# Performance work log

Hardware: AMD Instinct MI355X
Metric: run time of the kernel (lower is better)

The kernel has to match this reference:

```python
import jax, jax.numpy as jnp
import numpy as np

U_DIM = 2048
V_DIM = 2048
LATENT = 2048
BATCH = 8192
SLOPE = 0.001  # LeakyReLU negative slope
EPS = 1e-5     # torch LayerNorm default eps


def layer_norm(x, gamma, beta):
    mu = jnp.mean(x, axis=-1, keepdims=True)
    var = jnp.var(x, axis=-1, keepdims=True)
    return (x - mu) * jax.lax.rsqrt(var + EPS) * gamma + beta


def leaky_relu(x):
    return jnp.where(x >= 0, x, SLOPE * x)


def setup_inputs() -> dict:
    key = jax.random.key(0)
    ks = jax.random.split(key, 6)
    u = jax.random.normal(ks[0], (BATCH, V_DIM), dtype=jnp.float32)
    v = jax.random.normal(ks[1], (BATCH, U_DIM), dtype=jnp.float32)
    # LayerNorm affine params (torch default: weight=1, bias=0 at init; randomize slightly)
    ln_u_w = jnp.ones((V_DIM,), jnp.float32)
    ln_u_b = jnp.zeros((V_DIM,), jnp.float32)
    ln_v_w = jnp.ones((U_DIM,), jnp.float32)
    ln_v_b = jnp.zeros((U_DIM,), jnp.float32)
    # Linear params (Kaiming-uniform-like scale)
    su = 1.0 / np.sqrt(V_DIM)
    sv = 1.0 / np.sqrt(U_DIM)
    W_u = jax.random.uniform(ks[2], (V_DIM, LATENT), jnp.float32, -su, su)
    b_u = jax.random.uniform(ks[3], (LATENT,), jnp.float32, -su, su)
    W_v = jax.random.uniform(ks[4], (U_DIM, LATENT), jnp.float32, -sv, sv)
    b_v = jax.random.uniform(ks[5], (LATENT,), jnp.float32, -sv, sv)
    return {"u": u, "v": v, "ln_u_w": ln_u_w, "ln_u_b": ln_u_b,
            "ln_v_w": ln_v_w, "ln_v_b": ln_v_b,
            "W_u": W_u, "b_u": b_u, "W_v": W_v, "b_v": b_v}


def reference(u, v, ln_u_w, ln_u_b, ln_v_w, ln_v_b, W_u, b_u, W_v, b_v):
    # u tower: LayerNorm -> Linear -> LeakyReLU
    hu = leaky_relu(layer_norm(u, ln_u_w, ln_u_b) @ W_u + b_u)   # [B, latent]
    # v tower: LayerNorm -> Linear -> LeakyReLU
    hv = leaky_relu(layer_norm(v, ln_v_w, ln_v_b) @ W_v + b_v)   # [B, latent]
    # dot-product reduction per row
    return jnp.sum(hu * hv, axis=-1)                              # [B]
```

## Files before the change

kernel.cpp:

```cpp
#include <hip/hip_runtime.h>

typedef unsigned short u16;
typedef __attribute__((ext_vector_type(8))) short short8;
typedef __attribute__((ext_vector_type(16))) float f32x16;

#define DIM 2048
#define NROWS 8192
#define SLOPE 0.001f
#define LN_EPS 1e-5f

#define LN_BLOCKS 4096
#define WT_BLOCKS 2048

#define BM 128
#define BN 256
#define BK 64
#define NT (DIM / BK)

__device__ __forceinline__ u16 f2bf(float f) {
    unsigned int u = __float_as_uint(f);
    u += 0x7FFFu + ((u >> 16) & 1u);
    return (u16)(u >> 16);
}

__device__ __forceinline__ void gload_lds16(const void* g, void* l) {
    __builtin_amdgcn_global_load_lds(
        (const __attribute__((address_space(1))) void*)g,
        (__attribute__((address_space(3))) void*)l, 16, 0, 0);
}

__global__ __launch_bounds__(256) void prep_kernel(
    const float* __restrict__ u, const float* __restrict__ v,
    const float* __restrict__ lnu_w, const float* __restrict__ lnu_b,
    const float* __restrict__ lnv_w, const float* __restrict__ lnv_b,
    const float* __restrict__ Wu, const float* __restrict__ Wv,
    u16* __restrict__ Au, u16* __restrict__ Av,
    u16* __restrict__ WtU, u16* __restrict__ WtV)
{
    __shared__ u16 tile[64][66];

    if (blockIdx.x < LN_BLOCKS) {
        const int wave = threadIdx.x >> 6;
        const int lane = threadIdx.x & 63;
        const int r = blockIdx.x * 4 + wave;
        const bool isv = r >= NROWS;
        const int row = isv ? (r - NROWS) : r;
        const float* __restrict__ src = (isv ? v : u) + (size_t)row * DIM;
        const float* __restrict__ gw = isv ? lnv_w : lnu_w;
        const float* __restrict__ gb = isv ? lnv_b : lnu_b;
        u16* __restrict__ dst = (isv ? Av : Au) + (size_t)row * DIM;

        float4 x[8];
        #pragma unroll
        for (int i = 0; i < 8; ++i)
            x[i] = *(const float4*)(src + i * 256 + lane * 4);

        float s = 0.f, s2 = 0.f;
        #pragma unroll
        for (int i = 0; i < 8; ++i) {
            s  += (x[i].x + x[i].y) + (x[i].z + x[i].w);
            s2 += x[i].x*x[i].x + x[i].y*x[i].y + x[i].z*x[i].z + x[i].w*x[i].w;
        }
        #pragma unroll
        for (int m = 1; m < 64; m <<= 1) {
            s  += __shfl_xor(s, m);
            s2 += __shfl_xor(s2, m);
        }
        const float mu = s * (1.0f / DIM);
        const float rstd = rsqrtf(s2 * (1.0f / DIM) - mu * mu + LN_EPS);

        #pragma unroll
        for (int i = 0; i < 8; ++i) {
            const float4 w4 = *(const float4*)(gw + i * 256 + lane * 4);
            const float4 b4 = *(const float4*)(gb + i * 256 + lane * 4);
            union { u16 us[4]; uint2 v2; } pk;
            pk.us[0] = f2bf((x[i].x - mu) * rstd * w4.x + b4.x);
            pk.us[1] = f2bf((x[i].y - mu) * rstd * w4.y + b4.y);
            pk.us[2] = f2bf((x[i].z - mu) * rstd * w4.z + b4.z);
            pk.us[3] = f2bf((x[i].w - mu) * rstd * w4.w + b4.w);
            *(uint2*)(dst + i * 256 + lane * 4) = pk.v2;
        }
    } else {
        const int b = blockIdx.x - LN_BLOCKS;
        const int tower = b >> 10;
        const int t6 = b & 1023;
        const int n0 = (t6 & 31) * 64;
        const int k0 = (t6 >> 5) * 64;
        const float* __restrict__ src = tower ? Wv : Wu;
        u16* __restrict__ dst = tower ? WtV : WtU;
        const int c  = threadIdx.x & 15;
        const int rq = threadIdx.x >> 4;

        #pragma unroll
        for (int i = 0; i < 4; ++i) {
            const int k = rq + 16 * i;
            const float4 w = *(const float4*)(src + (size_t)(k0 + k) * DIM + n0 + c * 4);
            union { u16 us[4]; uint2 v2; } pk;
            pk.us[0] = f2bf(w.x); pk.us[1] = f2bf(w.y);
            pk.us[2] = f2bf(w.z); pk.us[3] = f2bf(w.w);
            *(uint2*)&tile[k][c * 4] = pk.v2;
        }
        __syncthreads();
        #pragma unroll
        for (int i = 0; i < 4; ++i) {
            const int n = rq + 16 * i;
            union { u16 us[4]; uint2 v2; } pk;
            #pragma unroll
            for (int j = 0; j < 4; ++j) pk.us[j] = tile[c * 4 + j][n];
            *(uint2*)(dst + (size_t)(n0 + n) * DIM + k0 + c * 4) = pk.v2;
        }
    }
}

__global__ __launch_bounds__(512) void fused_gemm_dot(
    const u16* __restrict__ Au, const u16* __restrict__ Av,
    const u16* __restrict__ WtU, const u16* __restrict__ WtV,
    const float* __restrict__ b_u, const float* __restrict__ b_v,
    float* __restrict__ out)
{
    __shared__ __align__(16) u16 smA[3][BM * BK];
    __shared__ __align__(16) u16 smB[3][BN * BK];

    const int tid   = threadIdx.x;
    const int wave  = tid >> 6;
    const int lane  = tid & 63;
    const int l31   = lane & 31;
    const int khalf = lane >> 5;
    const int wr    = wave >> 2;
    const int wc    = wave & 3;
    const int srow  = lane >> 3;
    const int gsw   = ((lane & 7) ^ srow ^ wave) * 8;

    const size_t arow0 = (size_t)blockIdx.x * BM;
    const size_t ncol0 = (size_t)blockIdx.y * BN;

#define STAGE(Asrc, Bsrc, k0, bi) do {                                             \
        _Pragma("unroll")                                                          \
        for (int i_ = 0; i_ < 2; ++i_) {                                           \
            const int rg_ = i_ * 64 + wave * 8;                                    \
            gload_lds16((Asrc) + (size_t)(rg_ + srow) * DIM + (k0) + gsw,          \
                        &smA[bi][rg_ * BK]);                                       \
        }                                                                          \
        _Pragma("unroll")                                                          \
        for (int i_ = 0; i_ < 4; ++i_) {                                           \
            const int rg_ = i_ * 64 + wave * 8;                                    \
            gload_lds16((Bsrc) + (size_t)(rg_ + srow) * DIM + (k0) + gsw,          \
                        &smB[bi][rg_ * BK]);                                       \
        }                                                                          \
    } while (0)

#define PHASE(bi, KS0) do {                                                        \
        const u16* sa_ = &smA[bi][0];                                              \
        const u16* sb_ = &smB[bi][0];                                              \
        short8 af_[2][2], bf_[2][2];                                               \
        _Pragma("unroll")                                                          \
        for (int kk_ = 0; kk_ < 2; ++kk_) {                                        \
            const int cb_ = ((KS0) + kk_) * 2 + khalf;                             \
            _Pragma("unroll")                                                      \
            for (int mi_ = 0; mi_ < 2; ++mi_) {                                    \
                const int row_ = wr * 64 + mi_ * 32 + l31;                         \
                const int sl_ = cb_ ^ (row_ & 7) ^ ((row_ >> 3) & 7);              \
                af_[mi_][kk_] = *(const short8*)(sa_ + row_ * BK + sl_ * 8);       \
            }                                                                      \
            _Pragma("unroll")                                                      \
            for (int ni_ = 0; ni_ < 2; ++ni_) {                                    \
                const int row_ = wc * 64 + ni_ * 32 + l31;                         \
                const int sl_ = cb_ ^ (row_ & 7) ^ ((row_ >> 3) & 7);              \
                bf_[ni_][kk_] = *(const short8*)(sb_ + row_ * BK + sl_ * 8);       \
            }                                                                      \
        }                                                                          \
        __builtin_amdgcn_s_setprio(1);                                             \
        _Pragma("unroll")                                                          \
        for (int kk_ = 0; kk_ < 2; ++kk_)                                          \
            _Pragma("unroll")                                                      \
            for (int mi_ = 0; mi_ < 2; ++mi_)                                      \
                _Pragma("unroll")                                                  \
                for (int ni_ = 0; ni_ < 2; ++ni_)                                  \
                    acc[mi_][ni_] = __builtin_amdgcn_mfma_f32_32x32x16_bf16(       \
                        af_[mi_][kk_], bf_[ni_][kk_], acc[mi_][ni_], 0, 0, 0);     \
        __builtin_amdgcn_s_setprio(0);                                             \
    } while (0)

    f32x16 acc[2][2];
    unsigned int hu_pk[2][2][8];

    #pragma unroll
    for (int tower = 0; tower < 2; ++tower) {
        const u16* __restrict__ Asrc = (tower ? Av : Au) + arow0 * DIM;
        const u16* __restrict__ Bsrc = (tower ? WtV : WtU) + ncol0 * DIM;

        #pragma unroll
        for (int mi = 0; mi < 2; ++mi)
            #pragma unroll
            for (int ni = 0; ni < 2; ++ni)
                #pragma unroll
                for (int r = 0; r < 16; ++r)
                    acc[mi][ni][r] = 0.f;

        STAGE(Asrc, Bsrc, 0, 0);
        STAGE(Asrc, Bsrc, BK, 1);

        int cur = 0;
        for (int t = 0; t < NT; ++t) {
            __builtin_amdgcn_sched_barrier(0);
            __builtin_amdgcn_s_barrier();
            __builtin_amdgcn_sched_barrier(0);
            if (t + 2 < NT) {
                int nb = cur + 2; if (nb >= 3) nb -= 3;
                STAGE(Asrc, Bsrc, (t + 2) * BK, nb);
                asm volatile("s_waitcnt vmcnt(12)" ::: "memory");
            } else if (t + 2 == NT) {
                asm volatile("s_waitcnt vmcnt(6)" ::: "memory");
            } else {
                asm volatile("s_waitcnt vmcnt(0)" ::: "memory");
            }
            __builtin_amdgcn_s_barrier();
            PHASE(cur, 0);
            __builtin_amdgcn_s_barrier();
            PHASE(cur, 2);
            cur = (cur == 2) ? 0 : cur + 1;
        }

        if (tower == 0) {
            #pragma unroll
            for (int ni = 0; ni < 2; ++ni) {
                const float bias = b_u[ncol0 + wc * 64 + ni * 32 + l31];
                #pragma unroll
                for (int mi = 0; mi < 2; ++mi) {
                    #pragma unroll
                    for (int p = 0; p < 8; ++p) {
                        float h0 = acc[mi][ni][p * 2] + bias;
                        float h1 = acc[mi][ni][p * 2 + 1] + bias;
                        h0 = h0 >= 0.f ? h0 : SLOPE * h0;
                        h1 = h1 >= 0.f ? h1 : SLOPE * h1;
                        hu_pk[mi][ni][p] = (unsigned)f2bf(h0) | ((unsigned)f2bf(h1) << 16);
                    }
                }
            }
        }
    }

    #pragma unroll
    for (int mi = 0; mi < 2; ++mi) {
        #pragma unroll
        for (int rg = 0; rg < 4; ++rg) {
            float rsum[4] = {0.f, 0.f, 0.f, 0.f};
            #pragma unroll
            for (int ni = 0; ni < 2; ++ni) {
                const float bias = b_v[ncol0 + wc * 64 + ni * 32 + l31];
                #pragma unroll
                for (int r = 0; r < 4; ++r) {
                    const int reg = rg * 4 + r;
                    float hv = acc[mi][ni][reg] + bias;
                    hv = hv >= 0.f ? hv : SLOPE * hv;
                    const unsigned pk = hu_pk[mi][ni][reg >> 1];
                    const unsigned bits = (reg & 1) ? (pk & 0xFFFF0000u) : (pk << 16);
                    rsum[r] += __uint_as_float(bits) * hv;
                }
            }
            #pragma unroll
            for (int r = 0; r < 4; ++r) {
                const int reg = rg * 4 + r;
                float vsum = rsum[r];
                vsum += __shfl_xor(vsum, 1);
                vsum += __shfl_xor(vsum, 2);
                vsum += __shfl_xor(vsum, 4);
                vsum += __shfl_xor(vsum, 8);
                vsum += __shfl_xor(vsum, 16);
                if (l31 == 0) {
                    const int row = (int)arow0 + wr * 64 + mi * 32
                                  + (reg & 3) + 8 * (reg >> 2) + 4 * khalf;
                    atomicAdd(out + row, vsum);
                }
            }
        }
    }
#undef STAGE
#undef PHASE
}

extern "C" void kernel_launch(void* const* d_in, const int* in_sizes, int n_in,
                              void* d_out, int out_size, void* d_ws, size_t ws_size,
                              hipStream_t stream)
{
    const float* u     = (const float*)d_in[0];
    const float* v     = (const float*)d_in[1];
    const float* lnu_w = (const float*)d_in[2];
    const float* lnu_b = (const float*)d_in[3];
    const float* lnv_w = (const float*)d_in[4];
    const float* lnv_b = (const float*)d_in[5];
    const float* W_u   = (const float*)d_in[6];
    const float* b_u   = (const float*)d_in[7];
    const float* W_v   = (const float*)d_in[8];
    const float* b_v   = (const float*)d_in[9];
    float* out = (float*)d_out;

    char* ws = (char*)d_ws;
    u16* Au  = (u16*)(ws);
    u16* Av  = (u16*)(ws + (size_t)NROWS * DIM * 2);
    u16* WtU = (u16*)(ws + (size_t)NROWS * DIM * 4);
    u16* WtV = (u16*)(ws + (size_t)NROWS * DIM * 4 + (size_t)DIM * DIM * 2);

    hipMemsetAsync(d_out, 0, (size_t)out_size * sizeof(float), stream);
    prep_kernel<<<LN_BLOCKS + WT_BLOCKS, 256, 0, stream>>>(
        u, v, lnu_w, lnu_b, lnv_w, lnv_b, W_u, W_v, Au, Av, WtU, WtV);
    fused_gemm_dot<<<dim3(NROWS / BM, DIM / BN), 512, 0, stream>>>(
        Au, Av, WtU, WtV, b_u, b_v, out);
}
```

Baseline: 368.3 us.

## Pipeline loads across both towers and fold output zeroing into prep kernel

The two tower K-loops now share one global tile index, so prefetches for the v tower start during the tail of the u tower and the pipeline never drains between towers. Global-to-LDS staging for the next tile is split into two halves and interleaved with the fragment reads and MFMA phases, and the waitcnt is simplified to a constant depth. The separate hipMemsetAsync of the output is removed; the prep kernel zeroes it instead, saving one launch. The risk is correctness at the tower boundary, since buffer rotation and the waitcnt counts must stay consistent with the staggered staging.

```diff
diff --git a/kernel.cpp b/kernel.cpp
--- a/kernel.cpp
+++ b/kernel.cpp
@@ -16,6 +16,7 @@
 #define BN 256
 #define BK 64
 #define NT (DIM / BK)
+#define TAUMAX (2 * NT)
 
 __device__ __forceinline__ u16 f2bf(float f) {
     unsigned int u = __float_as_uint(f);
@@ -35,9 +36,13 @@
     const float* __restrict__ lnv_w, const float* __restrict__ lnv_b,
     const float* __restrict__ Wu, const float* __restrict__ Wv,
     u16* __restrict__ Au, u16* __restrict__ Av,
-    u16* __restrict__ WtU, u16* __restrict__ WtV)
+    u16* __restrict__ WtU, u16* __restrict__ WtV,
+    float* __restrict__ out)
 {
     __shared__ u16 tile[64][66];
+
+    if (blockIdx.x < NROWS / 256)
+        out[(blockIdx.x << 8) | threadIdx.x] = 0.f;
 
     if (blockIdx.x < LN_BLOCKS) {
         const int wave = threadIdx.x >> 6;
@@ -134,61 +139,64 @@
     const size_t arow0 = (size_t)blockIdx.x * BM;
     const size_t ncol0 = (size_t)blockIdx.y * BN;
 
-#define STAGE(Asrc, Bsrc, k0, bi) do {                                             \
+#define STAGE_A(bi, tau) do {                                                      \
+        const u16* As_ = (((tau) >> 5) ? Av : Au) + arow0 * DIM + ((tau)&31)*BK;   \
         _Pragma("unroll")                                                          \
         for (int i_ = 0; i_ < 2; ++i_) {                                           \
             const int rg_ = i_ * 64 + wave * 8;                                    \
-            gload_lds16((Asrc) + (size_t)(rg_ + srow) * DIM + (k0) + gsw,          \
+            gload_lds16(As_ + (size_t)(rg_ + srow) * DIM + gsw,                    \
                         &smA[bi][rg_ * BK]);                                       \
         }                                                                          \
-        _Pragma("unroll")                                                          \
-        for (int i_ = 0; i_ < 4; ++i_) {                                           \
+    } while (0)
+
+#define STAGE_B(bi, tau, I0, I1) do {                                              \
+        const u16* Bs_ = (((tau) >> 5) ? WtV : WtU) + ncol0 * DIM + ((tau)&31)*BK; \
+        _Pragma("unroll")                                                          \
+        for (int i_ = (I0); i_ < (I1); ++i_) {                                     \
             const int rg_ = i_ * 64 + wave * 8;                                    \
-            gload_lds16((Bsrc) + (size_t)(rg_ + srow) * DIM + (k0) + gsw,          \
+            gload_lds16(Bs_ + (size_t)(rg_ + srow) * DIM + gsw,                    \
                         &smB[bi][rg_ * BK]);                                       \
         }                                                                          \
     } while (0)
 
-#define PHASE(bi, KS0) do {                                                        \
-        const u16* sa_ = &smA[bi][0];                                              \
-        const u16* sb_ = &smB[bi][0];                                              \
-        short8 af_[2][2], bf_[2][2];                                               \
-        _Pragma("unroll")                                                          \
-        for (int kk_ = 0; kk_ < 2; ++kk_) {                                        \
-            const int cb_ = ((KS0) + kk_) * 2 + khalf;                             \
-            _Pragma("unroll")                                                      \
-            for (int mi_ = 0; mi_ < 2; ++mi_) {                                    \
-                const int row_ = wr * 64 + mi_ * 32 + l31;                         \
-                const int sl_ = cb_ ^ (row_ & 7) ^ ((row_ >> 3) & 7);              \
-                af_[mi_][kk_] = *(const short8*)(sa_ + row_ * BK + sl_ * 8);       \
-            }                                                                      \
-            _Pragma("unroll")                                                      \
-            for (int ni_ = 0; ni_ < 2; ++ni_) {                                    \
-                const int row_ = wc * 64 + ni_ * 32 + l31;                         \
-                const int sl_ = cb_ ^ (row_ & 7) ^ ((row_ >> 3) & 7);              \
-                bf_[ni_][kk_] = *(const short8*)(sb_ + row_ * BK + sl_ * 8);       \
-            }                                                                      \
+#define LDFRAGS(sa_, sb_, KK, X) do {                                              \
+        const int cb_ = (KK) * 2 + khalf;                                          \
+        _Pragma("unroll")                                                          \
+        for (int mi_ = 0; mi_ < 2; ++mi_) {                                        \
+            const int row_ = wr * 64 + mi_ * 32 + l31;                             \
+            const int sl_ = cb_ ^ (row_ & 7) ^ ((row_ >> 3) & 7);                  \
+            af[mi_][X] = *(const short8*)((sa_) + row_ * BK + sl_ * 8);            \
         }                                                                          \
+        _Pragma("unroll")                                                          \
+        for (int ni_ = 0; ni_ < 2; ++ni_) {                                        \
+            const int row_ = wc * 64 + ni_ * 32 + l31;                             \
+            const int sl_ = cb_ ^ (row_ & 7) ^ ((row_ >> 3) & 7);                  \
+            bf[ni_][X] = *(const short8*)((sb_) + row_ * BK + sl_ * 8);            \
+        }                                                                          \
+    } while (0)
+
+#define MFMA8() do {                                                               \
         __builtin_amdgcn_s_setprio(1);                                             \
         _Pragma("unroll")                                                          \
-        for (int kk_ = 0; kk_ < 2; ++kk_)                                          \
+        for (int x_ = 0; x_ < 2; ++x_)                                             \
             _Pragma("unroll")                                                      \
             for (int mi_ = 0; mi_ < 2; ++mi_)                                      \
                 _Pragma("unroll")                                                  \
                 for (int ni_ = 0; ni_ < 2; ++ni_)                                  \
                     acc[mi_][ni_] = __builtin_amdgcn_mfma_f32_32x32x16_bf16(       \
-                        af_[mi_][kk_], bf_[ni_][kk_], acc[mi_][ni_], 0, 0, 0);     \
+                        af[mi_][x_], bf[ni_][x_], acc[mi_][ni_], 0, 0, 0);         \
         __builtin_amdgcn_s_setprio(0);                                             \
     } while (0)
 
     f32x16 acc[2][2];
     unsigned int hu_pk[2][2][8];
 
+    STAGE_A(0, 0); STAGE_B(0, 0, 0, 4);
+    STAGE_A(1, 1); STAGE_B(1, 1, 0, 4);
+
+    int cur = 0;
     #pragma unroll
     for (int tower = 0; tower < 2; ++tower) {
-        const u16* __restrict__ Asrc = (tower ? Av : Au) + arow0 * DIM;
-        const u16* __restrict__ Bsrc = (tower ? WtV : WtU) + ncol0 * DIM;
-
         #pragma unroll
         for (int mi = 0; mi < 2; ++mi)
             #pragma unroll
@@ -197,27 +205,31 @@
                 for (int r = 0; r < 16; ++r)
                     acc[mi][ni][r] = 0.f;
 
-        STAGE(Asrc, Bsrc, 0, 0);
-        STAGE(Asrc, Bsrc, BK, 1);
-
-        int cur = 0;
+        #pragma unroll 1
         for (int t = 0; t < NT; ++t) {
-            __builtin_amdgcn_sched_barrier(0);
+            const int tau = tower * NT + t;
+            if (tau == TAUMAX - 1) asm volatile("s_waitcnt vmcnt(0)" ::: "memory");
+            else                   asm volatile("s_waitcnt vmcnt(6)" ::: "memory");
             __builtin_amdgcn_s_barrier();
-            __builtin_amdgcn_sched_barrier(0);
-            if (t + 2 < NT) {
-                int nb = cur + 2; if (nb >= 3) nb -= 3;
-                STAGE(Asrc, Bsrc, (t + 2) * BK, nb);
-                asm volatile("s_waitcnt vmcnt(12)" ::: "memory");
-            } else if (t + 2 == NT) {
-                asm volatile("s_waitcnt vmcnt(6)" ::: "memory");
-            } else {
-                asm volatile("s_waitcnt vmcnt(0)" ::: "memory");
-            }
+            asm volatile("" ::: "memory");
+
+            const u16* sa = &smA[cur][0];
+            const u16* sb = &smB[cur][0];
+            int nb = cur + 2; if (nb >= 3) nb -= 3;
+            short8 af[2][2], bf[2][2];
+
+            LDFRAGS(sa, sb, 0, 0);
+            LDFRAGS(sa, sb, 1, 1);
+            if (tau + 2 < TAUMAX) { STAGE_A(nb, tau + 2); STAGE_B(nb, tau + 2, 0, 2); }
             __builtin_amdgcn_s_barrier();
-            PHASE(cur, 0);
+            MFMA8();
             __builtin_amdgcn_s_barrier();
-            PHASE(cur, 2);
+            LDFRAGS(sa, sb, 2, 0);
+            LDFRAGS(sa, sb, 3, 1);
+            if (tau + 2 < TAUMAX) STAGE_B(nb, tau + 2, 2, 4);
+            __builtin_amdgcn_s_barrier();
+            MFMA8();
+
             cur = (cur == 2) ? 0 : cur + 1;
         }
 
@@ -275,8 +287,10 @@
             }
         }
     }
-#undef STAGE
-#undef PHASE
+#undef STAGE_A
+#undef STAGE_B
+#undef LDFRAGS
+#undef MFMA8
 }
 
 extern "C" void kernel_launch(void* const* d_in, const int* in_sizes, int n_in,
@@ -301,9 +315,8 @@
     u16* WtU = (u16*)(ws + (size_t)NROWS * DIM * 4);
     u16* WtV = (u16*)(ws + (size_t)NROWS * DIM * 4 + (size_t)DIM * DIM * 2);
 
-    hipMemsetAsync(d_out, 0, (size_t)out_size * sizeof(float), stream);
     prep_kernel<<<LN_BLOCKS + WT_BLOCKS, 256, 0, stream>>>(
-        u, v, lnu_w, lnu_b, lnv_w, lnv_b, W_u, W_v, Au, Av, WtU, WtV);
+        u, v, lnu_w, lnu_b, lnv_w, lnv_b, W_u, W_v, Au, Av, WtU, WtV, out);
     fused_gemm_dot<<<dim3(NROWS / BM, DIM / BN), 512, 0, stream>>>(
         Au, Av, WtU, WtV, b_u, b_v, out);
 }
```

New measurement: 339.1 us, median of 2. -7.9%, faster.
